# Kernel optimization log

Measured on AMD Instinct MI355X. Metric: run time of the kernel, lower is better.

Reference implementation:

```python
import jax, jax.numpy as jnp
import numpy as np

FREQ_RES = 100.0 / 256.0
NUM_FILTERS = 6
_CFG = [(0.5, 4.0), (4.0, 8.0), (8.0, 12.0), (12.0, 16.0), (16.0, 24.0), (24.0, 30.0)]
BANDS = [(int(a / FREQ_RES), int(b / FREQ_RES)) for a, b in _CFG]  # (start_bin, end_bin)


def _interp_idx(n_src, n_dst):
    # torch F.interpolate bilinear, align_corners=False, along last dim (T dim is identity since same size)
    j = np.arange(n_dst)
    src = np.maximum((j + 0.5) * n_src / n_dst - 0.5, 0.0)
    x0 = np.floor(src).astype(np.int32)
    x1 = np.minimum(x0 + 1, n_src - 1)
    w = (src - x0).astype(np.float32)
    return x0, x1, w


def _gelu(x):
    return jax.nn.gelu(x, approximate=False)


def _forward(spec, centers, widths, gains, align_w, align_b, fc1_w, fc1_b, fc2_w, fc2_b,
             band_gain, gate_w, gate_b, proj_w, proj_b, bn_gamma, bn_beta, bn_mean, bn_var):
    B, C, T, F = spec.shape
    N = NUM_FILTERS
    band_feats = []
    for i, (s, e) in enumerate(BANDS):
        nb = e - s + 1
        sl = spec[:, :, :, s:e + 1]                       # [B,C,T,nb]
        mu = jax.nn.softplus(centers[i]) + s              # [C,N]
        mu = jnp.clip(mu, s, s + nb - 1)
        std = jnp.clip(jax.nn.softplus(widths[i]) + 1e-3, 0.5, 2.0 * nb / N)
        freqs = jnp.arange(nb, dtype=spec.dtype)          # relative bins [nb]
        g = jnp.exp(-0.5 * ((freqs[None, None, :] - mu[:, :, None]) / std[:, :, None]) ** 2)  # [C,N,nb]
        w = gains[i][:, :, None] * g / (g.sum(-1, keepdims=True) + 1e-6)
        filt = jnp.einsum('bctf,cnf->bctn', sl, w)        # [B,C,T,N]
        aligned = jnp.einsum('bctn,dc->bdtn', filt, align_w[i]) + align_b[i][None, :, None, None]
        band_feats.append(aligned)
    band_stack = jnp.stack(band_feats, axis=1)            # [B,6,C,T,N]
    nb_bands = band_stack.shape[1]
    x = band_stack.reshape(B, nb_bands * C, T, N)
    h = _gelu(jnp.einsum('bktn,ok->botn', x, fc1_w) + fc1_b[None, :, None, None])
    attn = jnp.einsum('botn,ko->bktn', h, fc2_w) + fc2_b[None, :, None, None]
    attn = jax.nn.softmax(attn.reshape(B, nb_bands, C, T, N), axis=1)  # softmax over bands
    band_stack = band_stack * attn * band_gain[None, :, None, None, None]
    enhanced = jnp.zeros_like(spec)
    for i, (s, e) in enumerate(BANDS):
        nb = e - s + 1
        narrow = band_stack[:, i]                         # [B,C,T,N]
        x0, x1, wl = _interp_idx(NUM_FILTERS, nb)
        wl = jnp.asarray(wl, dtype=spec.dtype)
        bf = narrow[..., x0] * (1.0 - wl) + narrow[..., x1] * wl   # [B,C,T,nb]
        enhanced = enhanced.at[:, :, :, s:e + 1].add(bf)
    residual = enhanced - spec
    gate = jax.nn.sigmoid(jnp.einsum('bctf,dc->bdtf', residual, gate_w) + gate_b[None, :, None, None])
    enhanced2 = spec + gate * residual
    y = jnp.einsum('bctf,dc->bdtf', enhanced2, proj_w) + proj_b[None, :, None, None]
    y = (y - bn_mean[None, :, None, None]) / jnp.sqrt(bn_var[None, :, None, None] + 1e-5)
    y = y * bn_gamma[None, :, None, None] + bn_beta[None, :, None, None]
    return _gelu(y)


def setup_inputs() -> dict:
    key = jax.random.key(0)
    ks = jax.random.split(key, 8)
    B, C, T, F, N = 64, 3, 3000, 103, NUM_FILTERS
    spec = jax.random.normal(ks[0], (B, C, T, F), dtype=jnp.float32)
    centers = jnp.stack([jnp.broadcast_to(jnp.linspace(a, b, N, dtype=jnp.float32) / FREQ_RES, (C, N)) for a, b in _CFG])
    widths = jnp.stack([jnp.full((C, N), (b - a) / N / FREQ_RES, dtype=jnp.float32) for a, b in _CFG])
    gains = jnp.ones((6, C, N), jnp.float32)
    align_w = jax.random.normal(ks[1], (6, C, C), dtype=jnp.float32) / np.sqrt(C)
    align_b = jax.random.normal(ks[2], (6, C), dtype=jnp.float32) * 0.02
    inter = 2 * C
    fc1_w = jax.random.normal(ks[3], (inter, 6 * C), dtype=jnp.float32) / np.sqrt(6 * C)
    fc1_b = jnp.zeros((inter,), jnp.float32)
    fc2_w = jax.random.normal(ks[4], (6 * C, inter), dtype=jnp.float32) / np.sqrt(inter)
    fc2_b = jnp.zeros((6 * C,), jnp.float32)
    band_gain = jnp.ones((6,), jnp.float32)
    gate_w = jax.random.normal(ks[5], (C, C), dtype=jnp.float32) / np.sqrt(C)
    gate_b = jnp.zeros((C,), jnp.float32)
    proj_w = jax.random.normal(ks[6], (C, C), dtype=jnp.float32) / np.sqrt(C)
    proj_b = jnp.zeros((C,), jnp.float32)
    bn_gamma = jnp.ones((C,), jnp.float32)
    bn_beta = jnp.zeros((C,), jnp.float32)
    bn_mean = jnp.zeros((C,), jnp.float32)
    bn_var = jnp.ones((C,), jnp.float32)
    return {"spec": spec, "centers": centers, "widths": widths, "gains": gains,
            "align_w": align_w, "align_b": align_b, "fc1_w": fc1_w, "fc1_b": fc1_b,
            "fc2_w": fc2_w, "fc2_b": fc2_b, "band_gain": band_gain,
            "gate_w": gate_w, "gate_b": gate_b, "proj_w": proj_w, "proj_b": proj_b,
            "bn_gamma": bn_gamma, "bn_beta": bn_beta, "bn_mean": bn_mean, "bn_var": bn_var}


def reference(spec, centers, widths, gains, align_w, align_b, fc1_w, fc1_b, fc2_w, fc2_b,
              band_gain, gate_w, gate_b, proj_w, proj_b, bn_gamma, bn_beta, bn_mean, bn_var):
    return _forward(spec, centers, widths, gains, align_w, align_b, fc1_w, fc1_b, fc2_w, fc2_b,
                    band_gain, gate_w, gate_b, proj_w, proj_b, bn_gamma, bn_beta, bn_mean, bn_var)
```

## Files before the change

kernel.cpp:

```cpp
#include <hip/hip_runtime.h>
#include <math.h>

namespace {

constexpr int C_ = 3, T_ = 3000, F_ = 103, NB_ = 6;
constexpr int TT = 20;
constexpr int NT = 5;
constexpr int BS[NB_]  = {1, 10, 20, 30, 40, 61};
constexpr int BNB[NB_] = {10, 11, 11, 11, 22, 16};
constexpr int BOF[NB_] = {0, 10, 21, 32, 43, 65};
constexpr int SPF = 81;
constexpr int PLANE = T_ * F_;
constexpr int SECP = 2064;
constexpr int WTOT = 1458;
constexpr int POOL2 = 6192;

__device__ __forceinline__ float softplus_(float x) {
  return fmaxf(x, 0.0f) + log1pf(expf(-fabsf(x)));
}
__device__ __forceinline__ float sigmoid_(float z) {
  return 1.0f / (1.0f + __expf(-z));
}
__device__ __forceinline__ float gelu_(float x) {
  return x * sigmoid_(1.595769122f * x * (1.0f + 0.044715f * x * x));
}

__global__ __launch_bounds__(128)
void prep_kernel(const float* __restrict__ centers,
                 const float* __restrict__ widths,
                 const float* __restrict__ gains,
                 const float* __restrict__ proj_w,
                 const float* __restrict__ proj_b,
                 const float* __restrict__ bn_gamma,
                 const float* __restrict__ bn_beta,
                 const float* __restrict__ bn_mean,
                 const float* __restrict__ bn_var,
                 float* __restrict__ ws)
{
  const int q = threadIdx.x;
  if (q < 108) {
    int i = q / 18;
    int p = q - i * 18;
    int s = BS[i], nb = BNB[i];
    float mu = softplus_(centers[q]) + (float)s;
    mu = fminf(fmaxf(mu, (float)s), (float)(s + nb - 1));
    float sd = softplus_(widths[q]) + 0.001f;
    sd = fminf(fmaxf(sd, 0.5f), 2.0f * (float)nb / 6.0f);
    float sum = 0.0f;
    for (int f = 0; f < nb; ++f) {
      float d = ((float)f - mu) / sd;
      sum += __expf(-0.5f * d * d);
    }
    float sc = gains[q] / (sum + 1e-6f);
    float* wrow = &ws[BOF[i] * 18 + p * nb];
    for (int f = 0; f < nb; ++f) {
      float d = ((float)f - mu) / sd;
      wrow[f] = sc * __expf(-0.5f * d * d);
    }
  } else if (q < 117) {
    int k = q - 108, d = k / 3;
    float sc = bn_gamma[d] / sqrtf(bn_var[d] + 1e-5f);
    ws[WTOT + k] = proj_w[k] * sc;
  } else if (q < 120) {
    int d = q - 117;
    float sc = bn_gamma[d] / sqrtf(bn_var[d] + 1e-5f);
    ws[WTOT + 9 + d] = (proj_b[d] - bn_mean[d]) * sc + bn_beta[d];
  }
}

__global__ __launch_bounds__(256)
void sleepband_kernel(const float* __restrict__ spec,
                      const float* __restrict__ ws,
                      const float* __restrict__ align_w,
                      const float* __restrict__ align_b,
                      const float* __restrict__ fc1_w,
                      const float* __restrict__ fc1_b,
                      const float* __restrict__ fc2_w,
                      const float* __restrict__ fc2_b,
                      const float* __restrict__ band_gain,
                      const float* __restrict__ gate_w,
                      const float* __restrict__ gate_b,
                      float* __restrict__ out)
{
  __shared__ __align__(16) float sPool[POOL2];
  __shared__ float sW[WTOT];
  __shared__ float sBand[TT][109];
  __shared__ float sAw[54], sAb[18], sF1[108], sF1b[6], sF2[108], sF2b[18],
                   sBg[6], sGw[9], sGb[3], sPw[9], sPb[3];

  const int tid = threadIdx.x;
  const int b   = blockIdx.y;
  const float* specB = spec + (size_t)b * C_ * PLANE;
  float* outBase = out + (size_t)b * C_ * PLANE;

  for (int k = tid; k < WTOT; k += 256) sW[k] = ws[k];
  if (tid < 54)  sAw[tid]  = align_w[tid];
  if (tid < 18)  sAb[tid]  = align_b[tid];
  if (tid < 108) sF1[tid]  = fc1_w[tid];
  if (tid < 6)   sF1b[tid] = fc1_b[tid];
  if (tid < 108) sF2[tid]  = fc2_w[tid];
  if (tid < 18)  sF2b[tid] = fc2_b[tid];
  if (tid < 6)   sBg[tid]  = band_gain[tid];
  if (tid < 9)   sGw[tid]  = gate_w[tid];
  if (tid < 3)   sGb[tid]  = gate_b[tid];
  if (tid < 9)   sPw[tid]  = ws[WTOT + tid];
  if (tid < 3)   sPb[tid]  = ws[WTOT + 9 + tid];

  for (int tile = 0; tile < NT; ++tile) {
    const int t0 = (blockIdx.x * NT + tile) * TT;

    for (int li = tid; li < C_ * TT * SPF; li += 256) {
      int c   = li / (TT * SPF);
      int rem = li - c * (TT * SPF);
      int tt  = rem / SPF;
      int f   = rem - tt * SPF;
      sPool[li] = specB[(size_t)c * PLANE + (size_t)(t0 + tt) * F_ + f];
    }
    __syncthreads();

    for (int task = tid; task < 18 * TT; task += 256) {
      int p  = task / TT;
      int tt = task - p * TT;
      int c  = p / 6;
      int n  = p - c * 6;
      const float* srowb = &sPool[(c * TT + tt) * SPF];
      #pragma unroll
      for (int i = 0; i < NB_; ++i) {
        const float* wrow = &sW[BOF[i] * 18 + p * BNB[i]];
        const float* srow = srowb + BS[i];
        float acc = 0.0f;
        #pragma unroll
        for (int f = 0; f < BNB[i]; ++f) acc += srow[f] * wrow[f];
        sBand[tt][(i * 3 + c) * 6 + n] = acc;
      }
    }
    __syncthreads();

    if (tid < 6 * TT) {
      int n  = tid / TT;
      int tt = tid - n * TT;
      float al[18];
      #pragma unroll
      for (int i = 0; i < 6; ++i) {
        float f0 = sBand[tt][(i * 3 + 0) * 6 + n];
        float f1 = sBand[tt][(i * 3 + 1) * 6 + n];
        float f2 = sBand[tt][(i * 3 + 2) * 6 + n];
        #pragma unroll
        for (int d = 0; d < 3; ++d)
          al[i * 3 + d] = sAw[i * 9 + d * 3 + 0] * f0 + sAw[i * 9 + d * 3 + 1] * f1 +
                          sAw[i * 9 + d * 3 + 2] * f2 + sAb[i * 3 + d];
      }
      float h[6];
      #pragma unroll
      for (int o = 0; o < 6; ++o) {
        float acc = sF1b[o];
        #pragma unroll
        for (int k = 0; k < 18; ++k) acc += sF1[o * 18 + k] * al[k];
        h[o] = gelu_(acc);
      }
      float at[18];
      #pragma unroll
      for (int k = 0; k < 18; ++k) {
        float acc = sF2b[k];
        #pragma unroll
        for (int o = 0; o < 6; ++o) acc += sF2[k * 6 + o] * h[o];
        at[k] = acc;
      }
      #pragma unroll
      for (int c = 0; c < 3; ++c) {
        float m = at[c];
        #pragma unroll
        for (int i = 1; i < 6; ++i) m = fmaxf(m, at[i * 3 + c]);
        float e[6], ssum = 0.0f;
        #pragma unroll
        for (int i = 0; i < 6; ++i) { e[i] = __expf(at[i * 3 + c] - m); ssum += e[i]; }
        float inv = 1.0f / ssum;
        #pragma unroll
        for (int i = 0; i < 6; ++i)
          sBand[tt][(i * 3 + c) * 6 + n] = al[i * 3 + c] * (e[i] * inv) * sBg[i];
      }
    }
    __syncthreads();

    if (tid < C_ * TT) {
      const int c  = tid / TT;
      const int tt = tid - c * TT;
      float bnd[36];
      #pragma unroll
      for (int i = 0; i < 6; ++i)
        #pragma unroll
        for (int n = 0; n < 6; ++n)
          bnd[i * 6 + n] = sBand[tt][(i * 3 + c) * 6 + n];
      float* row = &sPool[c * SECP + tt * F_];
      row[0] = 0.0f;
      float carry = 0.0f;
      #pragma unroll
      for (int i = 0; i < NB_; ++i) {
        #pragma unroll
        for (int j = 0; j < BNB[i]; ++j) {
          float src = ((float)j + 0.5f) * 6.0f / (float)BNB[i] - 0.5f;
          src = src > 0.0f ? src : 0.0f;
          int   x0 = (int)src;
          int   x1 = (x0 < 5) ? x0 + 1 : 5;
          float wl = src - (float)x0;
          float v  = bnd[i * 6 + x0] * (1.0f - wl) + bnd[i * 6 + x1] * wl;
          if (j == 0) v += carry;
          if (i < NB_ - 1 && j == BNB[i] - 1) carry = v;
          else row[BS[i] + j] = v;
        }
      }
      #pragma unroll
      for (int f = 77; f < F_; ++f) row[f] = 0.0f;
    }
    __syncthreads();

    float gw[9], pw[9], gb3[3], pb3[3];
    #pragma unroll
    for (int k = 0; k < 9; ++k) { gw[k] = sGw[k]; pw[k] = sPw[k]; }
    #pragma unroll
    for (int k = 0; k < 3; ++k) { gb3[k] = sGb[k]; pb3[k] = sPb[k]; }

    const float* sp0 = specB + (size_t)t0 * F_;
    float* outB = outBase + (size_t)t0 * F_;
    for (int e4 = tid; e4 < (TT * F_) / 4; e4 += 256) {
      const int e = e4 * 4;
      const float4 sA = *(const float4*)(sp0 + e);
      const float4 sB = *(const float4*)(sp0 + PLANE + e);
      const float4 sC = *(const float4*)(sp0 + 2 * PLANE + e);
      const float4 eA = *(const float4*)&sPool[0 * SECP + e];
      const float4 eB = *(const float4*)&sPool[1 * SECP + e];
      const float4 eC = *(const float4*)&sPool[2 * SECP + e];
      float4 oA, oB, oC;
      const float* sAp = (const float*)&sA; const float* sBp = (const float*)&sB;
      const float* sCp = (const float*)&sC;
      const float* eAp = (const float*)&eA; const float* eBp = (const float*)&eB;
      const float* eCp = (const float*)&eC;
      float* oAp = (float*)&oA; float* oBp = (float*)&oB; float* oCp = (float*)&oC;
      #pragma unroll
      for (int j = 0; j < 4; ++j) {
        float sv0 = sAp[j], sv1 = sBp[j], sv2 = sCp[j];
        float r0 = eAp[j] - sv0, r1 = eBp[j] - sv1, r2 = eCp[j] - sv2;
        float e20 = sv0 + sigmoid_(gw[0] * r0 + gw[1] * r1 + gw[2] * r2 + gb3[0]) * r0;
        float e21 = sv1 + sigmoid_(gw[3] * r0 + gw[4] * r1 + gw[5] * r2 + gb3[1]) * r1;
        float e22 = sv2 + sigmoid_(gw[6] * r0 + gw[7] * r1 + gw[8] * r2 + gb3[2]) * r2;
        float y0 = pw[0] * e20 + pw[1] * e21 + pw[2] * e22 + pb3[0];
        float y1 = pw[3] * e20 + pw[4] * e21 + pw[5] * e22 + pb3[1];
        float y2 = pw[6] * e20 + pw[7] * e21 + pw[8] * e22 + pb3[2];
        oAp[j] = gelu_(y0); oBp[j] = gelu_(y1); oCp[j] = gelu_(y2);
      }
      *(float4*)(outB + e) = oA;
      *(float4*)(outB + PLANE + e) = oB;
      *(float4*)(outB + 2 * PLANE + e) = oC;
    }
    __syncthreads();
  }
}

}

extern "C" void kernel_launch(void* const* d_in, const int* in_sizes, int n_in,
                              void* d_out, int out_size, void* d_ws, size_t ws_size,
                              hipStream_t stream) {
  (void)n_in; (void)out_size; (void)ws_size;
  const int B = in_sizes[0] / (C_ * T_ * F_);
  float* ws = (float*)d_ws;
  prep_kernel<<<1, 128, 0, stream>>>(
      (const float*)d_in[1],  (const float*)d_in[2],  (const float*)d_in[3],
      (const float*)d_in[13], (const float*)d_in[14], (const float*)d_in[15],
      (const float*)d_in[16], (const float*)d_in[17], (const float*)d_in[18], ws);
  dim3 grid(T_ / (TT * NT), B);
  sleepband_kernel<<<grid, 256, 0, stream>>>(
      (const float*)d_in[0],  ws,
      (const float*)d_in[4],  (const float*)d_in[5],
      (const float*)d_in[6],  (const float*)d_in[7],  (const float*)d_in[8],
      (const float*)d_in[9],  (const float*)d_in[10], (const float*)d_in[11],
      (const float*)d_in[12], (float*)d_out);
}
```

Baseline: 239.1 us.

## Pack band filter weights as bf16 pairs and compute two filters per thread

```diff
diff --git a/kernel.cpp b/kernel.cpp
--- a/kernel.cpp
+++ b/kernel.cpp
@@ -5,14 +5,16 @@
 
 constexpr int C_ = 3, T_ = 3000, F_ = 103, NB_ = 6;
 constexpr int TT = 20;
-constexpr int NT = 5;
+constexpr int NT = 3;
 constexpr int BS[NB_]  = {1, 10, 20, 30, 40, 61};
 constexpr int BNB[NB_] = {10, 11, 11, 11, 22, 16};
-constexpr int BOF[NB_] = {0, 10, 21, 32, 43, 65};
+constexpr int WB[NB_]  = {0, 5, 11, 17, 23, 34};
+constexpr int WBC[NB_] = {5, 6, 6, 6, 11, 8};
+constexpr int WROW = 42;
+constexpr int WTOTU = 18 * WROW;
 constexpr int SPF = 81;
 constexpr int PLANE = T_ * F_;
 constexpr int SECP = 2064;
-constexpr int WTOT = 1458;
 constexpr int POOL2 = 6192;
 
 __device__ __forceinline__ float softplus_(float x) {
@@ -23,6 +25,11 @@
 }
 __device__ __forceinline__ float gelu_(float x) {
   return x * sigmoid_(1.595769122f * x * (1.0f + 0.044715f * x * x));
+}
+__device__ __forceinline__ unsigned bf16_rne_(float x) {
+  unsigned b = __float_as_uint(x);
+  b += 0x7FFFu + ((b >> 16) & 1u);
+  return b >> 16;
 }
 
 __global__ __launch_bounds__(128)
@@ -37,6 +44,7 @@
                  const float* __restrict__ bn_var,
                  float* __restrict__ ws)
 {
+  unsigned* wsU = (unsigned*)ws;
   const int q = threadIdx.x;
   if (q < 108) {
     int i = q / 18;
@@ -52,19 +60,25 @@
       sum += __expf(-0.5f * d * d);
     }
     float sc = gains[q] / (sum + 1e-6f);
-    float* wrow = &ws[BOF[i] * 18 + p * nb];
+    float wtmp[22];
     for (int f = 0; f < nb; ++f) {
       float d = ((float)f - mu) / sd;
-      wrow[f] = sc * __expf(-0.5f * d * d);
+      wtmp[f] = sc * __expf(-0.5f * d * d);
+    }
+    const int wc = (nb + 1) / 2;
+    for (int e = 0; e < wc; ++e) {
+      unsigned lo = bf16_rne_(wtmp[2 * e]);
+      unsigned hi = (2 * e + 1 < nb) ? bf16_rne_(wtmp[2 * e + 1]) : 0u;
+      wsU[p * WROW + WB[i] + e] = lo | (hi << 16);
     }
   } else if (q < 117) {
     int k = q - 108, d = k / 3;
     float sc = bn_gamma[d] / sqrtf(bn_var[d] + 1e-5f);
-    ws[WTOT + k] = proj_w[k] * sc;
+    ws[WTOTU + k] = proj_w[k] * sc;
   } else if (q < 120) {
     int d = q - 117;
     float sc = bn_gamma[d] / sqrtf(bn_var[d] + 1e-5f);
-    ws[WTOT + 9 + d] = (proj_b[d] - bn_mean[d]) * sc + bn_beta[d];
+    ws[WTOTU + 9 + d] = (proj_b[d] - bn_mean[d]) * sc + bn_beta[d];
   }
 }
 
@@ -83,7 +97,7 @@
                       float* __restrict__ out)
 {
   __shared__ __align__(16) float sPool[POOL2];
-  __shared__ float sW[WTOT];
+  __shared__ unsigned sWu[WTOTU];
   __shared__ float sBand[TT][109];
   __shared__ float sAw[54], sAb[18], sF1[108], sF1b[6], sF2[108], sF2b[18],
                    sBg[6], sGw[9], sGb[3], sPw[9], sPb[3];
@@ -92,8 +106,9 @@
   const int b   = blockIdx.y;
   const float* specB = spec + (size_t)b * C_ * PLANE;
   float* outBase = out + (size_t)b * C_ * PLANE;
-
-  for (int k = tid; k < WTOT; k += 256) sW[k] = ws[k];
+  const unsigned* wsU = (const unsigned*)ws;
+
+  for (int k = tid; k < WTOTU; k += 256) sWu[k] = wsU[k];
   if (tid < 54)  sAw[tid]  = align_w[tid];
   if (tid < 18)  sAb[tid]  = align_b[tid];
   if (tid < 108) sF1[tid]  = fc1_w[tid];
@@ -103,8 +118,8 @@
   if (tid < 6)   sBg[tid]  = band_gain[tid];
   if (tid < 9)   sGw[tid]  = gate_w[tid];
   if (tid < 3)   sGb[tid]  = gate_b[tid];
-  if (tid < 9)   sPw[tid]  = ws[WTOT + tid];
-  if (tid < 3)   sPb[tid]  = ws[WTOT + 9 + tid];
+  if (tid < 9)   sPw[tid]  = ws[WTOTU + tid];
+  if (tid < 3)   sPb[tid]  = ws[WTOTU + 9 + tid];
 
   for (int tile = 0; tile < NT; ++tile) {
     const int t0 = (blockIdx.x * NT + tile) * TT;
@@ -118,20 +133,30 @@
     }
     __syncthreads();
 
-    for (int task = tid; task < 18 * TT; task += 256) {
-      int p  = task / TT;
-      int tt = task - p * TT;
-      int c  = p / 6;
-      int n  = p - c * 6;
-      const float* srowb = &sPool[(c * TT + tt) * SPF];
+    if (tid < 180) {
+      const int g  = tid / TT;
+      const int tt = tid - g * TT;
+      const int c  = g / 3;
+      const int np = g - c * 3;
+      const int n0 = 2 * np;
+      const float* srow = &sPool[(c * TT + tt) * SPF];
+      const unsigned* w0 = &sWu[(c * 6 + n0) * WROW];
+      const unsigned* w1 = w0 + WROW;
       #pragma unroll
       for (int i = 0; i < NB_; ++i) {
-        const float* wrow = &sW[BOF[i] * 18 + p * BNB[i]];
-        const float* srow = srowb + BS[i];
-        float acc = 0.0f;
-        #pragma unroll
-        for (int f = 0; f < BNB[i]; ++f) acc += srow[f] * wrow[f];
-        sBand[tt][(i * 3 + c) * 6 + n] = acc;
+        const float* sr = srow + BS[i];
+        float a0 = 0.0f, a1 = 0.0f;
+        #pragma unroll
+        for (int e = 0; e < WBC[i]; ++e) {
+          float s0 = sr[2 * e], s1 = sr[2 * e + 1];
+          unsigned u0 = w0[WB[i] + e], u1 = w1[WB[i] + e];
+          a0 += s0 * __uint_as_float(u0 << 16);
+          a0 += s1 * __uint_as_float(u0 & 0xffff0000u);
+          a1 += s0 * __uint_as_float(u1 << 16);
+          a1 += s1 * __uint_as_float(u1 & 0xffff0000u);
+        }
+        sBand[tt][(i * 3 + c) * 6 + n0]     = a0;
+        sBand[tt][(i * 3 + c) * 6 + n0 + 1] = a1;
       }
     }
     __syncthreads();
```

Measured after the change: 239.8 us. Within noise of the previous version (+0.3%).
